# Kernel optimization log

Hardware: AMD Instinct MI355X
Metric: run time of the kernel (lower is better)

The kernel has to match this reference:

```python
import jax, jax.numpy as jnp
import numpy as np

B, S, D, H = 4, 2048, 512, 8
HD = D // H  # head dim = 64
NEG = 1e9


def setup_inputs() -> dict:
    key = jax.random.key(0)
    ks = jax.random.split(key, 10)
    x = jax.random.normal(ks[0], (B, S, D), dtype=jnp.float32)
    group_ids = jnp.sort(jax.random.randint(ks[1], (B, S), 0, 8), axis=-1)
    s = 0.05
    Wq = jax.random.normal(ks[2], (D, D), dtype=jnp.float32) * s
    Wk = jax.random.normal(ks[3], (D, D), dtype=jnp.float32) * s
    Wv = jax.random.normal(ks[4], (D, D), dtype=jnp.float32) * s
    Wo = jax.random.normal(ks[5], (D, D), dtype=jnp.float32) * s
    bq = jnp.zeros((D,), jnp.float32)
    bk = jnp.zeros((D,), jnp.float32)
    bv = jnp.zeros((D,), jnp.float32)
    bo = jnp.zeros((D,), jnp.float32)
    return {"x": x, "group_ids": group_ids, "Wq": Wq, "bq": bq,
            "Wk": Wk, "bk": bk, "Wv": Wv, "bv": bv, "Wo": Wo, "bo": bo}


def reference(x, group_ids, Wq, bq, Wk, bk, Wv, bv, Wo, bo):
    relu = jax.nn.relu
    # projections + activation (activation='relu' is applied to q,k,v AND output)
    q = relu(x @ Wq + bq)  # [B,S,D]
    k = relu(x @ Wk + bk)
    v = relu(x @ Wv + bv)
    # split heads -> [B,H,S,HD]
    def split(t):
        return t.reshape(B, S, H, HD).transpose(0, 2, 1, 3)
    qh, kh, vh = split(q), split(k), split(v)
    # note: scale uses feature dim AFTER head split, i.e. head_dim
    scale = 1.0 / jnp.sqrt(jnp.float32(HD))
    e = jnp.einsum('bhqd,bhkd->bhqk', qh, kh) * scale  # [B,H,S,S]
    group_mask = (group_ids[:, None, :, None] == group_ids[:, None, None, :])  # [B,1,S,S]
    e = e - (1.0 - group_mask.astype(jnp.float32)) * NEG
    a = jax.nn.softmax(e, axis=-1)
    yh = jnp.einsum('bhqk,bhkd->bhqd', a, vh)  # [B,H,S,HD]
    y = yh.transpose(0, 2, 1, 3).reshape(B, S, D)
    return relu(y @ Wo + bo)
```

## Files before the change

### kernel.cpp

```cpp
#include <hip/hip_runtime.h>
#include <cmath>

#define Bsz 4
#define Ssz 2048
#define Dsz 512
#define Hn 8

typedef unsigned short u16;
typedef _Float16 f16;
typedef __attribute__((ext_vector_type(4))) _Float16 f16x4;
typedef __attribute__((ext_vector_type(8))) _Float16 f16x8;
typedef __attribute__((ext_vector_type(8))) unsigned short us8;
typedef __attribute__((ext_vector_type(4))) float f32x4;
typedef __attribute__((ext_vector_type(16))) float f32x16;

__device__ __forceinline__ void gl2lds16(const void* g, void* l) {
    __builtin_amdgcn_global_load_lds(
        (const __attribute__((address_space(1))) void*)g,
        (__attribute__((address_space(3))) void*)l, 16, 0, 0);
}

__global__ __launch_bounds__(256) void prep(const float* __restrict__ x,
                                            f16* __restrict__ xb,
                                            const float* __restrict__ Wq,
                                            const float* __restrict__ Wk,
                                            const float* __restrict__ Wv,
                                            const float* __restrict__ Wo,
                                            f16* __restrict__ Wtqkv,
                                            f16* __restrict__ Wto) {
    const int blk = blockIdx.x;
    const int tid = threadIdx.x;
    if (blk < 2048) {
        int i = blk * 256 + tid;
        const float4* xv = (const float4*)x;
        float4 a = xv[2 * i], b = xv[2 * i + 1];
        f16x8 o;
        o[0] = (f16)a.x; o[1] = (f16)a.y; o[2] = (f16)a.z; o[3] = (f16)a.w;
        o[4] = (f16)b.x; o[5] = (f16)b.y; o[6] = (f16)b.z; o[7] = (f16)b.w;
        ((f16x8*)xb)[i] = o;
        return;
    }
    __shared__ float T[64][65];
    const int bz = blk - 2048;
    const int z = bz >> 6;
    const int n0 = (bz & 7) * 64, k0 = ((bz >> 3) & 7) * 64;
    const float* W = (z == 0) ? Wq : (z == 1) ? Wk : (z == 2) ? Wv : Wo;
#pragma unroll
    for (int i = 0; i < 16; i++) {
        int e = tid + i * 256;
        int r = e >> 6, c = e & 63;
        T[r][c] = W[(size_t)(k0 + r) * Dsz + n0 + c];
    }
    __syncthreads();
    f16* dst = (z < 3) ? (Wtqkv + ((size_t)z * 512 + n0) * Dsz + k0)
                       : (Wto + (size_t)n0 * Dsz + k0);
#pragma unroll
    for (int i = 0; i < 16; i++) {
        int e = tid + i * 256;
        int r = e >> 6, c = e & 63;
        dst[(size_t)r * Dsz + c] = (f16)(T[c][r]);
    }
}

template <int MODE>
__global__ __launch_bounds__(256) void gemm128(
    const f16* __restrict__ A, const f16* __restrict__ Bt,
    f16* o0, f16* o1, u16* o2v,
    const float* b0, const float* b1, const float* b2,
    float* ofp, const float* bias_f) {
    __shared__ __align__(16) u16 smem[2 * 128 * 64];
    u16* As = smem;
    u16* Bs = smem + 128 * 64;
    const int tid = threadIdx.x;
    const int colg0 = blockIdx.x * 128;
    const int row0 = blockIdx.y * 128;
    const int w = tid >> 6, lane = tid & 63;
    const int nn = lane & 31, hh = lane >> 5;
    const int wr = w >> 1, wc = w & 1;

    f32x16 acc[2][2];
#pragma unroll
    for (int bi = 0; bi < 2; bi++)
#pragma unroll
        for (int bj = 0; bj < 2; bj++)
#pragma unroll
            for (int e = 0; e < 16; e++) acc[bi][bj][e] = 0.f;

    const f16* Ablk = A + (size_t)row0 * 512;
    const f16* Bblk = Bt + (size_t)colg0 * 512;

    for (int k0 = 0; k0 < 512; k0 += 64) {
        __syncthreads();
#pragma unroll
        for (int i = 0; i < 4; i++) {
            int p = tid + i * 256;
            int m = p >> 3, kc = p & 7;
            int gk = ((kc ^ (m & 7)) << 3);
            gl2lds16(Ablk + (size_t)m * 512 + k0 + gk, As + p * 8);
            gl2lds16(Bblk + (size_t)m * 512 + k0 + gk, Bs + p * 8);
        }
        __syncthreads();
#pragma unroll
        for (int t = 0; t < 4; t++) {
            f16x8 af[2], bfr[2];
#pragma unroll
            for (int bi = 0; bi < 2; bi++) {
                int r = wr * 64 + bi * 32 + nn;
                int ch = r * 8 + ((t * 2 + hh) ^ (r & 7));
                af[bi] = *(const f16x8*)(As + ch * 8);
            }
#pragma unroll
            for (int bj = 0; bj < 2; bj++) {
                int n = wc * 64 + bj * 32 + nn;
                int ch = n * 8 + ((t * 2 + hh) ^ (n & 7));
                bfr[bj] = *(const f16x8*)(Bs + ch * 8);
            }
#pragma unroll
            for (int bi = 0; bi < 2; bi++)
#pragma unroll
                for (int bj = 0; bj < 2; bj++)
                    acc[bi][bj] = __builtin_amdgcn_mfma_f32_32x32x16_f16(
                        af[bi], bfr[bj], acc[bi][bj], 0, 0, 0);
        }
    }

    if (MODE == 0) {
        const int sel = colg0 >> 9;
        const int c0 = colg0 & 511;
        if (sel < 2) {
            f16* outp = (sel == 0) ? o0 : o1;
            const float* bp = (sel == 0) ? b0 : b1;
#pragma unroll
            for (int bj = 0; bj < 2; bj++) {
                int col = c0 + wc * 64 + bj * 32 + nn;
                float bv = bp[col];
#pragma unroll
                for (int bi = 0; bi < 2; bi++)
#pragma unroll
                    for (int rg = 0; rg < 16; rg++) {
                        int row = row0 + wr * 64 + bi * 32 +
                                  (rg & 3) + 8 * (rg >> 2) + 4 * hh;
                        outp[(size_t)row * 512 + col] =
                            (f16)fmaxf(acc[bi][bj][rg] + bv, 0.f);
                    }
            }
        } else {
            const int hh_head = c0 >> 6;
            f16 (*T)[136] = (f16(*)[136])smem;
            const int bb = row0 >> 11;
            const int t0 = (row0 & 2047) >> 6;
            __syncthreads();
#pragma unroll
            for (int ph = 0; ph < 2; ph++) {
                if (wc == ph) {
#pragma unroll
                    for (int bj = 0; bj < 2; bj++) {
                        int d = bj * 32 + nn;
                        float bv = b2[c0 + ph * 64 + d];
#pragma unroll
                        for (int bi = 0; bi < 2; bi++)
#pragma unroll
                            for (int rg = 0; rg < 16; rg++) {
                                int s = wr * 64 + bi * 32 +
                                        (rg & 3) + 8 * (rg >> 2) + 4 * hh;
                                T[d][s] = (f16)fmaxf(acc[bi][bj][rg] + bv, 0.f);
                            }
                    }
                }
                __syncthreads();
#pragma unroll
                for (int ii = 0; ii < 4; ii++) {
                    int oct = tid + ii * 256;
                    int tt = oct >> 9, rem = oct & 511;
                    int d = rem >> 3, s8 = rem & 7;
                    us8 val = *(const us8*)(&T[d][tt * 64 + s8 * 8]);
                    size_t dst = (((size_t)((bb * 8 + hh_head + ph) * 32 + t0 + tt)) << 12)
                                 + d * 64 + s8 * 8;
                    *(us8*)(o2v + dst) = val;
                }
                __syncthreads();
            }
        }
    } else {
#pragma unroll
        for (int bj = 0; bj < 2; bj++) {
            int col = colg0 + wc * 64 + bj * 32 + nn;
            float bv = bias_f[col];
#pragma unroll
            for (int bi = 0; bi < 2; bi++)
#pragma unroll
                for (int rg = 0; rg < 16; rg++) {
                    int row = row0 + wr * 64 + bi * 32 +
                              (rg & 3) + 8 * (rg >> 2) + 4 * hh;
                    ofp[(size_t)row * 512 + col] = fmaxf(acc[bi][bj][rg] + bv, 0.f);
                }
        }
    }
}

__global__ __launch_bounds__(512) void attn_mfma(
    const f16* __restrict__ Q, const f16* __restrict__ K,
    const u16* __restrict__ VT, const int* __restrict__ G,
    f16* __restrict__ Y) {
    __shared__ __align__(16) u16 Ks[2][4096];
    __shared__ __align__(16) u16 Vs[2][4096];

    const int qt = blockIdx.x, h = blockIdx.y, b = blockIdx.z;
    const int q0 = qt * 128;
    const int tid = threadIdx.x;
    const int w = tid >> 6, lane = tid & 63;
    const int ln = lane & 15, quad = lane >> 4;

    const f16* Qb = Q + (size_t)b * Ssz * Dsz;
    const f16* Kb = K + (size_t)b * Ssz * Dsz;
    const u16* Vtb = VT + (size_t)(b * Hn + h) * 32 * 4096;
    const int* Gb = G + (size_t)b * Ssz;

    f16x8 qf[2];
    {
        const f16* qrow = Qb + (size_t)(q0 + w * 16 + ln) * Dsz + h * 64;
        qf[0] = *(const f16x8*)(qrow + quad * 8);
        qf[1] = *(const f16x8*)(qrow + 32 + quad * 8);
    }
    const int gq = Gb[q0 + w * 16 + ln];
    const int gqmin = Gb[q0], gqmax = Gb[q0 + 127];

    int gf = 0, gl = 0; bool ov = false;
    if (lane < 32) {
        gf = Gb[lane * 64]; gl = Gb[lane * 64 + 63];
        ov = (gl >= gqmin) && (gf <= gqmax);
    }
    unsigned long long mask = __ballot(ov);
    const int kt_lo = __builtin_ctzll(mask);
    const int kt_hi = 63 - __builtin_clzll(mask);

    f32x4 o[4];
    const f32x4 z4 = {0.f, 0.f, 0.f, 0.f};
#pragma unroll
    for (int nd = 0; nd < 4; nd++) o[nd] = z4;
    float lsum = 0.f;

#define STAGE_K(kt, bi_)                                                       \
    {                                                                          \
        const f16* Ktile = Kb + (size_t)(kt) * 64 * Dsz + h * 64;              \
        int row = tid >> 3, c = tid & 7;                                       \
        gl2lds16(Ktile + (size_t)row * Dsz + ((c ^ (row & 7)) << 3),           \
                 Ks[bi_] + tid * 8);                                           \
    }
#define STAGE_V(kt, bi_)                                                       \
    {                                                                          \
        const u16* Vtile = Vtb + (size_t)(kt) * 4096;                          \
        int row = tid >> 3, c = tid & 7;                                       \
        gl2lds16(Vtile + row * 64 + ((c ^ (row & 7)) << 3),                    \
                 Vs[bi_] + tid * 8);                                           \
    }

    STAGE_K(kt_lo, 0)
    STAGE_V(kt_lo, 0)

    int buf = 0;
    for (int kt = kt_lo; kt <= kt_hi; kt++) {
        __syncthreads();
        if (kt < kt_hi) { STAGE_K(kt + 1, buf ^ 1) STAGE_V(kt + 1, buf ^ 1) }
        const u16* ks = Ks[buf];
        const u16* vs = Vs[buf];
        const int k0 = kt * 64;
        const int gkf = __shfl(gf, kt), gkl = __shfl(gl, kt);
        const bool needMask = !(gqmin == gqmax && gkf == gkl);

        f16x4 pf[4];
#pragma unroll
        for (int kb = 0; kb < 4; kb++) {
            f32x4 s = z4;
#pragma unroll
            for (int kk = 0; kk < 2; kk++) {
                int key = kb * 16 + ln;
                int ch = key * 8 + ((kk * 4 + quad) ^ (key & 7));
                f16x8 kf = *(const f16x8*)(ks + ch * 8);
                s = __builtin_amdgcn_mfma_f32_16x16x32_f16(kf, qf[kk], s, 0, 0, 0);
            }
            float sv[4];
            if (needMask) {
                int4 g4 = *(const int4*)(Gb + k0 + kb * 16 + quad * 4);
                sv[0] = (gq == g4.x) ? s[0] * 0.125f - 4.0f : -1e9f;
                sv[1] = (gq == g4.y) ? s[1] * 0.125f - 4.0f : -1e9f;
                sv[2] = (gq == g4.z) ? s[2] * 0.125f - 4.0f : -1e9f;
                sv[3] = (gq == g4.w) ? s[3] * 0.125f - 4.0f : -1e9f;
            } else {
#pragma unroll
                for (int r = 0; r < 4; r++) sv[r] = s[r] * 0.125f - 4.0f;
            }
            f16x4 pp;
#pragma unroll
            for (int r = 0; r < 4; r++) {
                float e = __expf(sv[r]);
                lsum += e;
                pp[r] = (f16)e;
            }
            pf[kb] = pp;
        }
#pragma unroll
        for (int nd = 0; nd < 4; nd++)
#pragma unroll
            for (int kc = 0; kc < 4; kc++) {
                int addr = (((nd * 16 + ln) * 8 +
                             ((kc * 2 + (quad >> 1)) ^ (ln & 7))) << 3) +
                           (quad & 1) * 4;
                f16x4 vf = *(const f16x4*)(vs + addr);
                o[nd] = __builtin_amdgcn_mfma_f32_16x16x16f16(pf[kc], vf, o[nd], 0, 0, 0);
            }
        buf ^= 1;
    }

    lsum += __shfl_xor(lsum, 16);
    lsum += __shfl_xor(lsum, 32);
    float linv = 1.0f / lsum;
#pragma unroll
    for (int r = 0; r < 4; r++) {
        float lr = __shfl(linv, (lane & 48) | (quad * 4 + r));
        size_t row = (size_t)b * Ssz + q0 + w * 16 + quad * 4 + r;
#pragma unroll
        for (int nd = 0; nd < 4; nd++)
            Y[row * Dsz + h * 64 + nd * 16 + ln] = (f16)(o[nd][r] * lr);
    }
#undef STAGE_K
#undef STAGE_V
}

extern "C" void kernel_launch(void* const* d_in, const int* in_sizes, int n_in,
                              void* d_out, int out_size, void* d_ws, size_t ws_size,
                              hipStream_t stream) {
    const float* x  = (const float*)d_in[0];
    const int*   g  = (const int*)d_in[1];
    const float* Wq = (const float*)d_in[2];
    const float* bq = (const float*)d_in[3];
    const float* Wk = (const float*)d_in[4];
    const float* bk = (const float*)d_in[5];
    const float* Wv = (const float*)d_in[6];
    const float* bv = (const float*)d_in[7];
    const float* Wo = (const float*)d_in[8];
    const float* bo = (const float*)d_in[9];
    float* out = (float*)d_out;

    const size_t E = (size_t)Bsz * Ssz * Dsz;
    f16* xb  = (f16*)d_ws;
    f16* qb  = xb + E;
    f16* kb2 = qb + E;
    u16* vtb = (u16*)(kb2 + E);
    f16* yb  = (f16*)(vtb + E);
    f16* Wtqkv = yb + E;
    f16* Wto   = Wtqkv + 1536 * 512;

    prep<<<2304, 256, 0, stream>>>(x, xb, Wq, Wk, Wv, Wo, Wtqkv, Wto);
    gemm128<0><<<dim3(12, 64), 256, 0, stream>>>(xb, Wtqkv, qb, kb2, vtb,
                                                 bq, bk, bv, nullptr, nullptr);
    attn_mfma<<<dim3(Ssz / 128, Hn, Bsz), 512, 0, stream>>>(qb, kb2, vtb, g, yb);
    gemm128<1><<<dim3(4, 64), 256, 0, stream>>>(yb, Wto, nullptr, nullptr, nullptr,
                                                nullptr, nullptr, nullptr, out, bo);
}
```

Baseline: 150.5 us.

## Fold softmax scale into Wq and stage K in per-head tile layout

The 1/sqrt(hd) scale is folded into Wq during weight prep and into bq in the epilogue, which removes a multiply per score in attention. The QKV GEMM epilogue now goes through LDS for all three outputs. It writes Q with coalesced 16-byte stores and K in a contiguous per-head 64x64 tile layout like V. Attention then loads K tiles from contiguous 8KB blocks instead of strided rows. This adds LDS round trips and barriers in the GEMM epilogue for Q and K, and scaling Q before the fp16 cast slightly changes rounding.

```diff
diff --git a/kernel.cpp b/kernel.cpp
--- a/kernel.cpp
+++ b/kernel.cpp
@@ -45,6 +45,7 @@
     const int z = bz >> 6;
     const int n0 = (bz & 7) * 64, k0 = ((bz >> 3) & 7) * 64;
     const float* W = (z == 0) ? Wq : (z == 1) ? Wk : (z == 2) ? Wv : Wo;
+    const float sc = (z == 0) ? 0.125f : 1.0f;
 #pragma unroll
     for (int i = 0; i < 16; i++) {
         int e = tid + i * 256;
@@ -58,14 +59,14 @@
     for (int i = 0; i < 16; i++) {
         int e = tid + i * 256;
         int r = e >> 6, c = e & 63;
-        dst[(size_t)r * Dsz + c] = (f16)(T[c][r]);
+        dst[(size_t)r * Dsz + c] = (f16)(T[c][r] * sc);
     }
 }
 
 template <int MODE>
 __global__ __launch_bounds__(256) void gemm128(
     const f16* __restrict__ A, const f16* __restrict__ Bt,
-    f16* o0, f16* o1, u16* o2v,
+    u16* o0, u16* o1, u16* o2v,
     const float* b0, const float* b1, const float* b2,
     float* ofp, const float* bias_f) {
     __shared__ __align__(16) u16 smem[2 * 128 * 64];
@@ -127,59 +128,60 @@
     if (MODE == 0) {
         const int sel = colg0 >> 9;
         const int c0 = colg0 & 511;
-        if (sel < 2) {
-            f16* outp = (sel == 0) ? o0 : o1;
-            const float* bp = (sel == 0) ? b0 : b1;
-#pragma unroll
-            for (int bj = 0; bj < 2; bj++) {
-                int col = c0 + wc * 64 + bj * 32 + nn;
-                float bv = bp[col];
-#pragma unroll
-                for (int bi = 0; bi < 2; bi++)
-#pragma unroll
-                    for (int rg = 0; rg < 16; rg++) {
-                        int row = row0 + wr * 64 + bi * 32 +
-                                  (rg & 3) + 8 * (rg >> 2) + 4 * hh;
-                        outp[(size_t)row * 512 + col] =
-                            (f16)fmaxf(acc[bi][bj][rg] + bv, 0.f);
-                    }
-            }
-        } else {
-            const int hh_head = c0 >> 6;
-            f16 (*T)[136] = (f16(*)[136])smem;
-            const int bb = row0 >> 11;
-            const int t0 = (row0 & 2047) >> 6;
+        const float bscale = (sel == 0) ? 0.125f : 1.0f;
+        const float* bp = (sel == 0) ? b0 : (sel == 1) ? b1 : b2;
+        u16* outp = (sel == 0) ? o0 : (sel == 1) ? o1 : o2v;
+        const int bb = row0 >> 11;
+        const int t0 = (row0 & 2047) >> 6;
+        f16 (*Tv)[136] = (f16(*)[136])smem;
+        f16 (*Tq)[72]  = (f16(*)[72])smem;
+        __syncthreads();
+#pragma unroll
+        for (int ph = 0; ph < 2; ph++) {
+            if (wc == ph) {
+#pragma unroll
+                for (int bj = 0; bj < 2; bj++) {
+                    int cl = bj * 32 + nn;
+                    float bv = bp[c0 + ph * 64 + cl] * bscale;
+#pragma unroll
+                    for (int bi = 0; bi < 2; bi++)
+#pragma unroll
+                        for (int rg = 0; rg < 16; rg++) {
+                            int row = wr * 64 + bi * 32 +
+                                      (rg & 3) + 8 * (rg >> 2) + 4 * hh;
+                            f16 v = (f16)fmaxf(acc[bi][bj][rg] + bv, 0.f);
+                            if (sel == 2) Tv[cl][row] = v;
+                            else          Tq[row][cl] = v;
+                        }
+                }
+            }
             __syncthreads();
-#pragma unroll
-            for (int ph = 0; ph < 2; ph++) {
-                if (wc == ph) {
-#pragma unroll
-                    for (int bj = 0; bj < 2; bj++) {
-                        int d = bj * 32 + nn;
-                        float bv = b2[c0 + ph * 64 + d];
-#pragma unroll
-                        for (int bi = 0; bi < 2; bi++)
-#pragma unroll
-                            for (int rg = 0; rg < 16; rg++) {
-                                int s = wr * 64 + bi * 32 +
-                                        (rg & 3) + 8 * (rg >> 2) + 4 * hh;
-                                T[d][s] = (f16)fmaxf(acc[bi][bj][rg] + bv, 0.f);
-                            }
+            const int head = (c0 >> 6) + ph;
+#pragma unroll
+            for (int ii = 0; ii < 4; ii++) {
+                int idx = tid + ii * 256;
+                us8 val;
+                size_t dst;
+                if (sel == 2) {
+                    int tt = idx >> 9, rem = idx & 511;
+                    int d = rem >> 3, s8 = rem & 7;
+                    val = *(const us8*)(&Tv[d][tt * 64 + s8 * 8]);
+                    dst = (((size_t)((bb * 8 + head) * 32 + t0 + tt)) << 12)
+                          + d * 64 + s8 * 8;
+                } else {
+                    int row = idx >> 3, s8 = idx & 7;
+                    val = *(const us8*)(&Tq[row][s8 * 8]);
+                    if (sel == 0) {
+                        dst = (size_t)(row0 + row) * 512 + c0 + ph * 64 + s8 * 8;
+                    } else {
+                        int tt = row >> 6, i2 = row & 63;
+                        dst = (((size_t)((bb * 8 + head) * 32 + t0 + tt)) << 12)
+                              + i2 * 64 + s8 * 8;
                     }
                 }
-                __syncthreads();
-#pragma unroll
-                for (int ii = 0; ii < 4; ii++) {
-                    int oct = tid + ii * 256;
-                    int tt = oct >> 9, rem = oct & 511;
-                    int d = rem >> 3, s8 = rem & 7;
-                    us8 val = *(const us8*)(&T[d][tt * 64 + s8 * 8]);
-                    size_t dst = (((size_t)((bb * 8 + hh_head + ph) * 32 + t0 + tt)) << 12)
-                                 + d * 64 + s8 * 8;
-                    *(us8*)(o2v + dst) = val;
-                }
-                __syncthreads();
-            }
+                *(us8*)(outp + dst) = val;
+            }
+            __syncthreads();
         }
     } else {
 #pragma unroll
@@ -199,7 +201,7 @@
 }
 
 __global__ __launch_bounds__(512) void attn_mfma(
-    const f16* __restrict__ Q, const f16* __restrict__ K,
+    const f16* __restrict__ Q, const u16* __restrict__ KP,
     const u16* __restrict__ VT, const int* __restrict__ G,
     f16* __restrict__ Y) {
     __shared__ __align__(16) u16 Ks[2][4096];
@@ -212,7 +214,7 @@
     const int ln = lane & 15, quad = lane >> 4;
 
     const f16* Qb = Q + (size_t)b * Ssz * Dsz;
-    const f16* Kb = K + (size_t)b * Ssz * Dsz;
+    const u16* Ktb = KP + (size_t)(b * Hn + h) * 32 * 4096;
     const u16* Vtb = VT + (size_t)(b * Hn + h) * 32 * 4096;
     const int* Gb = G + (size_t)b * Ssz;
 
@@ -240,28 +242,24 @@
     for (int nd = 0; nd < 4; nd++) o[nd] = z4;
     float lsum = 0.f;
 
-#define STAGE_K(kt, bi_)                                                       \
+#define STAGE_T(base, kt, dstbuf)                                              \
     {                                                                          \
-        const f16* Ktile = Kb + (size_t)(kt) * 64 * Dsz + h * 64;              \
+        const u16* tile = (base) + (size_t)(kt) * 4096;                        \
         int row = tid >> 3, c = tid & 7;                                       \
-        gl2lds16(Ktile + (size_t)row * Dsz + ((c ^ (row & 7)) << 3),           \
-                 Ks[bi_] + tid * 8);                                           \
-    }
-#define STAGE_V(kt, bi_)                                                       \
-    {                                                                          \
-        const u16* Vtile = Vtb + (size_t)(kt) * 4096;                          \
-        int row = tid >> 3, c = tid & 7;                                       \
-        gl2lds16(Vtile + row * 64 + ((c ^ (row & 7)) << 3),                    \
-                 Vs[bi_] + tid * 8);                                           \
-    }
-
-    STAGE_K(kt_lo, 0)
-    STAGE_V(kt_lo, 0)
+        gl2lds16(tile + row * 64 + ((c ^ (row & 7)) << 3),                     \
+                 (dstbuf) + tid * 8);                                          \
+    }
+
+    STAGE_T(Ktb, kt_lo, Ks[0])
+    STAGE_T(Vtb, kt_lo, Vs[0])
 
     int buf = 0;
     for (int kt = kt_lo; kt <= kt_hi; kt++) {
         __syncthreads();
-        if (kt < kt_hi) { STAGE_K(kt + 1, buf ^ 1) STAGE_V(kt + 1, buf ^ 1) }
+        if (kt < kt_hi) {
+            STAGE_T(Ktb, kt + 1, Ks[buf ^ 1])
+            STAGE_T(Vtb, kt + 1, Vs[buf ^ 1])
+        }
         const u16* ks = Ks[buf];
         const u16* vs = Vs[buf];
         const int k0 = kt * 64;
@@ -282,13 +280,13 @@
             float sv[4];
             if (needMask) {
                 int4 g4 = *(const int4*)(Gb + k0 + kb * 16 + quad * 4);
-                sv[0] = (gq == g4.x) ? s[0] * 0.125f - 4.0f : -1e9f;
-                sv[1] = (gq == g4.y) ? s[1] * 0.125f - 4.0f : -1e9f;
-                sv[2] = (gq == g4.z) ? s[2] * 0.125f - 4.0f : -1e9f;
-                sv[3] = (gq == g4.w) ? s[3] * 0.125f - 4.0f : -1e9f;
+                sv[0] = (gq == g4.x) ? s[0] - 4.0f : -1e9f;
+                sv[1] = (gq == g4.y) ? s[1] - 4.0f : -1e9f;
+                sv[2] = (gq == g4.z) ? s[2] - 4.0f : -1e9f;
+                sv[3] = (gq == g4.w) ? s[3] - 4.0f : -1e9f;
             } else {
 #pragma unroll
-                for (int r = 0; r < 4; r++) sv[r] = s[r] * 0.125f - 4.0f;
+                for (int r = 0; r < 4; r++) sv[r] = s[r] - 4.0f;
             }
             f16x4 pp;
 #pragma unroll
@@ -323,8 +321,7 @@
         for (int nd = 0; nd < 4; nd++)
             Y[row * Dsz + h * 64 + nd * 16 + ln] = (f16)(o[nd][r] * lr);
     }
-#undef STAGE_K
-#undef STAGE_V
+#undef STAGE_T
 }
 
 extern "C" void kernel_launch(void* const* d_in, const int* in_sizes, int n_in,
@@ -345,16 +342,17 @@
     const size_t E = (size_t)Bsz * Ssz * Dsz;
     f16* xb  = (f16*)d_ws;
     f16* qb  = xb + E;
-    f16* kb2 = qb + E;
-    u16* vtb = (u16*)(kb2 + E);
+    u16* kpb = (u16*)(qb + E);
+    u16* vtb = kpb + E;
     f16* yb  = (f16*)(vtb + E);
     f16* Wtqkv = yb + E;
     f16* Wto   = Wtqkv + 1536 * 512;
 
     prep<<<2304, 256, 0, stream>>>(x, xb, Wq, Wk, Wv, Wo, Wtqkv, Wto);
-    gemm128<0><<<dim3(12, 64), 256, 0, stream>>>(xb, Wtqkv, qb, kb2, vtb,
+    gemm128<0><<<dim3(12, 64), 256, 0, stream>>>(xb, Wtqkv, (u16*)qb, kpb, vtb,
                                                  bq, bk, bv, nullptr, nullptr);
-    attn_mfma<<<dim3(Ssz / 128, Hn, Bsz), 512, 0, stream>>>(qb, kb2, vtb, g, yb);
+    attn_mfma<<<dim3(Ssz / 128, Hn, Bsz), 512, 0, stream>>>(qb, kpb, vtb, g, yb);
     gemm128<1><<<dim3(4, 64), 256, 0, stream>>>(yb, Wto, nullptr, nullptr, nullptr,
-                                                nullptr, nullptr, nullptr, out, bo);
-}
+                                                nullptr, nullptr, nullptr,
+                                                out, bo);
+}
```

Measured after the change: 157.5 us. 4.7% more time.
